# Kernel tuning notes

Measured on AMD Instinct MI355X. Metric: run time of the kernel, lower is better.

## Reference

```python
import jax, jax.numpy as jnp
import numpy as np
from jax import lax

# Topology constants (windowed DAG: compute node i, at global index N_IN+i,
# reads the FANIN immediately preceding global node values).
N_IN = 16      # number of input nodes
FANIN = 16     # connections per compute node
N_NODES = 512  # topologically ordered compute nodes (hidden + output)
N_OUT = 64     # last N_OUT nodes in node_order are outputs
BATCH = 32768
T = N_IN + N_NODES  # total node count


def setup_inputs() -> dict:
    key = jax.random.key(0)
    k1, k2, k3, k4 = jax.random.split(key, 4)
    x = jax.random.normal(k1, (BATCH, N_IN), dtype=jnp.float32)
    # weights scaled down so tanh is not fully saturated through 512 layers
    weights = jax.random.normal(k2, (N_NODES, FANIN), dtype=jnp.float32) * 0.25
    biases = jax.random.normal(k3, (N_NODES,), dtype=jnp.float32) * 0.1
    responses = 1.0 + 0.1 * jax.random.normal(k4, (N_NODES,), dtype=jnp.float32)
    # src indices for node i: global indices [i, i+FANIN) (== previous FANIN nodes,
    # since N_IN == FANIN). Shape [N_NODES, FANIN], int32, all in [0, T).
    src_idx = (jnp.arange(N_NODES, dtype=jnp.int32)[:, None]
               + jnp.arange(FANIN, dtype=jnp.int32)[None, :]
               + (N_IN - FANIN))
    return {"x": x, "weights": weights, "biases": biases,
            "responses": responses, "src_idx": src_idx}


def _forward(x, weights, biases, responses, src_idx):
    B = x.shape[0]
    # values buffer [B, T]: inputs first, then compute nodes in topo order
    values0 = jnp.zeros((B, T), dtype=x.dtype).at[:, :N_IN].set(x)

    def body(values, xs):
        i, idx_row, w, b, r = xs
        src_vals = jnp.take(values, idx_row, axis=1)        # [B, FANIN] gather
        agg = src_vals @ w                                   # [B] weighted sum
        out = jnp.tanh(agg + b) * r                          # activation
        values = lax.dynamic_update_slice(values, out[:, None], (0, N_IN + i))
        return values, None

    ii = jnp.arange(N_NODES, dtype=jnp.int32)
    values, _ = lax.scan(body, values0, (ii, src_idx, weights, biases, responses))
    return values[:, T - N_OUT:]  # [B, N_OUT]


def reference(x, weights, biases, responses, src_idx):
    return _forward(x, weights, biases, responses, src_idx)
```

## Files before the change

kernel.cpp:

```cpp
#include <hip/hip_runtime.h>


typedef float v4f __attribute__((ext_vector_type(4)));

constexpr int kNodes  = 512;
constexpr int kNOut   = 64;
constexpr int kBatch  = 32768;
constexpr int kStrideF = 20;
constexpr int kLdsFloats = (kNodes + 3) * kStrideF + 4;
constexpr float kScale = 2.8853900817779268f;

#define PREF(S) {                                                             \
    asm volatile(                                                             \
      "ds_read_b128 %0, %5 offset:0\n\t"                                      \
      "ds_read_b128 %1, %5 offset:16\n\t"                                     \
      "ds_read_b128 %2, %5 offset:32\n\t"                                     \
      "ds_read_b128 %3, %5 offset:48\n\t"                                     \
      "ds_read_b128 %4, %5 offset:64"                                         \
      : "=&v"(q0[S]), "=&v"(q1[S]), "=&v"(q2[S]), "=&v"(q3[S]), "=&v"(q4[S])  \
      : "v"(a));                                                              \
    a += kStrideF * 4; }

#define WAITQ(S)                                                              \
    asm volatile("s_waitcnt lgkmcnt(15)"                                      \
      : "+v"(q0[S]), "+v"(q1[S]), "+v"(q2[S]), "+v"(q3[S]), "+v"(q4[S]));

#define NODE(K, A0,A1,A2,A3,A4,A5,A6,A7,A8,A9,A10,A11,A12,A13,A14,A15) {     \
    PREF(((K)+3)&3)                                                          \
    WAITQ((K)&3)                                                             \
    const int s = (K)&3;                                                     \
    v4f qa = q0[s], qb = q1[s], qc = q2[s], qd = q3[s], qm = q4[s];          \
    float p0 = fmaf(A0,  qa.x, qm.x);                                        \
    float p1 = A4  * qb.x;                                                   \
    float p2 = A8  * qc.x;                                                   \
    float p3 = A12 * qd.x;                                                   \
    p0 = fmaf(A1,  qa.y, p0);  p1 = fmaf(A5,  qb.y, p1);                     \
    p2 = fmaf(A9,  qc.y, p2);  p3 = fmaf(A13, qd.y, p3);                     \
    p0 = fmaf(A2,  qa.z, p0);  p1 = fmaf(A6,  qb.z, p1);                     \
    p2 = fmaf(A10, qc.z, p2);  p3 = fmaf(A14, qd.z, p3);                     \
    p0 = fmaf(A3,  qa.w, p0);  p1 = fmaf(A7,  qb.w, p1);                     \
    p2 = fmaf(A11, qc.w, p2);                                                \
    float pre = (p0 + p1) + (p2 + p3);                                       \
    float acc = fmaf(A15, qd.w, pre);          \
    float e = __builtin_amdgcn_exp2f(acc);                                   \
    float u = __builtin_amdgcn_rcpf(e + 1.0f);                               \
    A0 = fmaf(qm.z, u, qm.y); }

__global__ __launch_bounds__(128) void neat_fwd(
    const float* __restrict__ x,
    const float* __restrict__ w,
    const float* __restrict__ bias,
    const float* __restrict__ resp,
    float* __restrict__ out)
{
    __shared__ float lds[kLdsFloats];

    const int t = threadIdx.x;

    const float4* __restrict__ w4 = reinterpret_cast<const float4*>(w);
    #pragma unroll
    for (int j = 0; j < 16; ++j) {
        int i4 = t + j * 128;
        float4 v = w4[i4];
        int node = i4 >> 2, pos = (i4 & 3) << 2;
        float4 s = make_float4(v.x * kScale, v.y * kScale, v.z * kScale, v.w * kScale);
        *reinterpret_cast<float4*>(lds + node * kStrideF + pos) = s;
    }
    #pragma unroll
    for (int j = 0; j < 4; ++j) {
        int n = t + j * 128;
        float b = bias[n], r = resp[n];
        lds[n * kStrideF + 16] = b * kScale;
        lds[n * kStrideF + 17] = r;
        lds[n * kStrideF + 18] = -2.0f * r;
        lds[n * kStrideF + 19] = 0.0f;
    }

    const int b = blockIdx.x * blockDim.x + t;
    const float4* __restrict__ x4 = reinterpret_cast<const float4*>(x) + (size_t)b * 4;
    float4 a0 = x4[0], a1 = x4[1], a2 = x4[2], a3 = x4[3];
    float v0  = a0.x, v1  = a0.y, v2  = a0.z, v3  = a0.w;
    float v4  = a1.x, v5  = a1.y, v6  = a1.z, v7  = a1.w;
    float v8  = a2.x, v9  = a2.y, v10 = a2.z, v11 = a2.w;
    float v12 = a3.x, v13 = a3.y, v14 = a3.z, v15 = a3.w;

    float* __restrict__ op = out + (size_t)b * kNOut;

    __syncthreads();

    unsigned int a = (unsigned int)(unsigned long long)(&lds[0]);

    v4f q0[4], q1[4], q2[4], q3[4], q4[4];
    PREF(0) PREF(1) PREF(2)

    #pragma unroll 1
    for (int g = 0; g < 32; ++g) {
        NODE( 0, v0 ,v1 ,v2 ,v3 ,v4 ,v5 ,v6 ,v7 ,v8 ,v9 ,v10,v11,v12,v13,v14,v15)
        NODE( 1, v1 ,v2 ,v3 ,v4 ,v5 ,v6 ,v7 ,v8 ,v9 ,v10,v11,v12,v13,v14,v15,v0 )
        NODE( 2, v2 ,v3 ,v4 ,v5 ,v6 ,v7 ,v8 ,v9 ,v10,v11,v12,v13,v14,v15,v0 ,v1 )
        NODE( 3, v3 ,v4 ,v5 ,v6 ,v7 ,v8 ,v9 ,v10,v11,v12,v13,v14,v15,v0 ,v1 ,v2 )
        NODE( 4, v4 ,v5 ,v6 ,v7 ,v8 ,v9 ,v10,v11,v12,v13,v14,v15,v0 ,v1 ,v2 ,v3 )
        NODE( 5, v5 ,v6 ,v7 ,v8 ,v9 ,v10,v11,v12,v13,v14,v15,v0 ,v1 ,v2 ,v3 ,v4 )
        NODE( 6, v6 ,v7 ,v8 ,v9 ,v10,v11,v12,v13,v14,v15,v0 ,v1 ,v2 ,v3 ,v4 ,v5 )
        NODE( 7, v7 ,v8 ,v9 ,v10,v11,v12,v13,v14,v15,v0 ,v1 ,v2 ,v3 ,v4 ,v5 ,v6 )
        NODE( 8, v8 ,v9 ,v10,v11,v12,v13,v14,v15,v0 ,v1 ,v2 ,v3 ,v4 ,v5 ,v6 ,v7 )
        NODE( 9, v9 ,v10,v11,v12,v13,v14,v15,v0 ,v1 ,v2 ,v3 ,v4 ,v5 ,v6 ,v7 ,v8 )
        NODE(10, v10,v11,v12,v13,v14,v15,v0 ,v1 ,v2 ,v3 ,v4 ,v5 ,v6 ,v7 ,v8 ,v9 )
        NODE(11, v11,v12,v13,v14,v15,v0 ,v1 ,v2 ,v3 ,v4 ,v5 ,v6 ,v7 ,v8 ,v9 ,v10)
        NODE(12, v12,v13,v14,v15,v0 ,v1 ,v2 ,v3 ,v4 ,v5 ,v6 ,v7 ,v8 ,v9 ,v10,v11)
        NODE(13, v13,v14,v15,v0 ,v1 ,v2 ,v3 ,v4 ,v5 ,v6 ,v7 ,v8 ,v9 ,v10,v11,v12)
        NODE(14, v14,v15,v0 ,v1 ,v2 ,v3 ,v4 ,v5 ,v6 ,v7 ,v8 ,v9 ,v10,v11,v12,v13)
        NODE(15, v15,v0 ,v1 ,v2 ,v3 ,v4 ,v5 ,v6 ,v7 ,v8 ,v9 ,v10,v11,v12,v13,v14)
        if (g >= 28) {
            float4* o4 = reinterpret_cast<float4*>(op + (g - 28) * 16);
            o4[0] = make_float4(v0,  v1,  v2,  v3);
            o4[1] = make_float4(v4,  v5,  v6,  v7);
            o4[2] = make_float4(v8,  v9,  v10, v11);
            o4[3] = make_float4(v12, v13, v14, v15);
        }
    }

    asm volatile("s_waitcnt lgkmcnt(0)" ::: "memory");
}

extern "C" void kernel_launch(void* const* d_in, const int* in_sizes, int n_in,
                              void* d_out, int out_size, void* d_ws, size_t ws_size,
                              hipStream_t stream) {
    const float* x    = (const float*)d_in[0];
    const float* w    = (const float*)d_in[1];
    const float* bias = (const float*)d_in[2];
    const float* resp = (const float*)d_in[3];
    float* out = (float*)d_out;
    dim3 block(128);
    dim3 grid(kBatch / 128);
    hipLaunchKernelGGL(neat_fwd, grid, block, 0, stream, x, w, bias, resp, out);
}
```

Before: 99.88 us.

## Split each batch row across four lanes with DPP reductions and folded response scaling

Each batch element is now handled by a quad of four lanes, each holding 4 of the 16 sliding-window values and computing a partial dot product. The partials are combined with DPP quad permutes, and the window is rotated across lanes with a DPP shift. Response factors are folded into the downstream weights in LDS, and the final outputs are rescaled by the response at store time. This gives four times as many threads and more latency hiding per row, at the cost of a per-node cross-lane reduction and redundant exp/rcp work in every lane of the quad.

```diff
diff --git a/kernel.cpp b/kernel.cpp
--- a/kernel.cpp
+++ b/kernel.cpp
@@ -3,120 +3,121 @@
 
 typedef float v4f __attribute__((ext_vector_type(4)));
 
-constexpr int kNodes  = 512;
-constexpr int kNOut   = 64;
-constexpr int kBatch  = 32768;
-constexpr int kStrideF = 20;
-constexpr int kLdsFloats = (kNodes + 3) * kStrideF + 4;
-constexpr float kScale = 2.8853900817779268f;
+constexpr int kNOut     = 64;
+constexpr int kBatch    = 32768;
+constexpr int kQStrideF = 80;
+constexpr int kLdsFloats = (128 + 3) * kQStrideF;
+constexpr float kScale  = 2.8853900817779268f;
 
-#define PREF(S) {                                                             \
+#define QPERM(X, CTRL) __int_as_float(__builtin_amdgcn_update_dpp(            \
+    __float_as_int(X), __float_as_int(X), (CTRL), 0xF, 0xF, false))
+
+#define PREFQ(S) {                                                            \
     asm volatile(                                                             \
       "ds_read_b128 %0, %5 offset:0\n\t"                                      \
-      "ds_read_b128 %1, %5 offset:16\n\t"                                     \
-      "ds_read_b128 %2, %5 offset:32\n\t"                                     \
-      "ds_read_b128 %3, %5 offset:48\n\t"                                     \
-      "ds_read_b128 %4, %5 offset:64"                                         \
-      : "=&v"(q0[S]), "=&v"(q1[S]), "=&v"(q2[S]), "=&v"(q3[S]), "=&v"(q4[S])  \
+      "ds_read_b128 %1, %5 offset:64\n\t"                                     \
+      "ds_read_b128 %2, %5 offset:128\n\t"                                    \
+      "ds_read_b128 %3, %5 offset:192\n\t"                                    \
+      "ds_read_b128 %4, %5 offset:256"                                        \
+      : "=&v"(qw0[S]), "=&v"(qw1[S]), "=&v"(qw2[S]), "=&v"(qw3[S]),           \
+        "=&v"(qb[S])                                                          \
       : "v"(a));                                                              \
-    a += kStrideF * 4; }
+    a += kQStrideF * 4; }
 
 #define WAITQ(S)                                                              \
     asm volatile("s_waitcnt lgkmcnt(15)"                                      \
-      : "+v"(q0[S]), "+v"(q1[S]), "+v"(q2[S]), "+v"(q3[S]), "+v"(q4[S]));
+      : "+v"(qw0[S]), "+v"(qw1[S]), "+v"(qw2[S]), "+v"(qw3[S]), "+v"(qb[S]));
 
-#define NODE(K, A0,A1,A2,A3,A4,A5,A6,A7,A8,A9,A10,A11,A12,A13,A14,A15) {     \
-    PREF(((K)+3)&3)                                                          \
-    WAITQ((K)&3)                                                             \
-    const int s = (K)&3;                                                     \
-    v4f qa = q0[s], qb = q1[s], qc = q2[s], qd = q3[s], qm = q4[s];          \
-    float p0 = fmaf(A0,  qa.x, qm.x);                                        \
-    float p1 = A4  * qb.x;                                                   \
-    float p2 = A8  * qc.x;                                                   \
-    float p3 = A12 * qd.x;                                                   \
-    p0 = fmaf(A1,  qa.y, p0);  p1 = fmaf(A5,  qb.y, p1);                     \
-    p2 = fmaf(A9,  qc.y, p2);  p3 = fmaf(A13, qd.y, p3);                     \
-    p0 = fmaf(A2,  qa.z, p0);  p1 = fmaf(A6,  qb.z, p1);                     \
-    p2 = fmaf(A10, qc.z, p2);  p3 = fmaf(A14, qd.z, p3);                     \
-    p0 = fmaf(A3,  qa.w, p0);  p1 = fmaf(A7,  qb.w, p1);                     \
-    p2 = fmaf(A11, qc.w, p2);                                                \
-    float pre = (p0 + p1) + (p2 + p3);                                       \
-    float acc = fmaf(A15, qd.w, pre);          \
-    float e = __builtin_amdgcn_exp2f(acc);                                   \
-    float u = __builtin_amdgcn_rcpf(e + 1.0f);                               \
-    A0 = fmaf(qm.z, u, qm.y); }
+#define NODE1(QW, BSV, WA, WB, WC, WD) {                                      \
+    float ini = is_l0 ? (BSV) : 0.0f;                                         \
+    float p = fmaf((WA), (QW).x, ini);                                        \
+    p = fmaf((WB), (QW).y, p);                                                \
+    p = fmaf((WC), (QW).z, p);                                                \
+    p = fmaf((WD), (QW).w, p);                                                \
+    float s1 = p + QPERM(p, 0xB1);                   \
+    float sf = s1 + QPERM(s1, 0x4E);                 \
+    float ex = __builtin_amdgcn_exp2f(sf);                                    \
+    float uu = __builtin_amdgcn_rcpf(ex + 1.0f);                              \
+    float tn = fmaf(-2.0f, uu, 1.0f);             \
+    float mg = QPERM((WA), 0x39);                    \
+    (WA) = is_l3 ? tn : mg; }
 
-__global__ __launch_bounds__(128) void neat_fwd(
+#define NODEQ(S) {                                                            \
+    PREFQ(((S) + 3) & 3)                                                      \
+    WAITQ(S)                                                                  \
+    v4f f0 = qw0[S], f1 = qw1[S], f2 = qw2[S], f3 = qw3[S], fb = qb[S];       \
+    NODE1(f0, fb.x, r0, r1, r2, r3)                                           \
+    NODE1(f1, fb.y, r1, r2, r3, r0)                                           \
+    NODE1(f2, fb.z, r2, r3, r0, r1)                                           \
+    NODE1(f3, fb.w, r3, r0, r1, r2) }
+
+__global__ __launch_bounds__(512) void neat_fwd(
     const float* __restrict__ x,
     const float* __restrict__ w,
     const float* __restrict__ bias,
     const float* __restrict__ resp,
     float* __restrict__ out)
 {
-    __shared__ float lds[kLdsFloats];
+    __shared__ alignas(16) float ldsw[kLdsFloats];
+    __shared__ float rst[512];
 
-    const int t = threadIdx.x;
+    const int t  = threadIdx.x;
+    const int jl = t & 3;
+    const bool is_l0 = (jl == 0);
+    const bool is_l3 = (jl == 3);
+
+    rst[t] = resp[t];
+    __syncthreads();
 
     const float4* __restrict__ w4 = reinterpret_cast<const float4*>(w);
     #pragma unroll
-    for (int j = 0; j < 16; ++j) {
-        int i4 = t + j * 128;
+    for (int k = 0; k < 4; ++k) {
+        int i4 = t + k * 512;
         float4 v = w4[i4];
-        int node = i4 >> 2, pos = (i4 & 3) << 2;
-        float4 s = make_float4(v.x * kScale, v.y * kScale, v.z * kScale, v.w * kScale);
-        *reinterpret_cast<float4*>(lds + node * kStrideF + pos) = s;
+        int n = i4 >> 2, k4 = i4 & 3;
+        int s0 = n + 4 * k4;
+        float f0 = kScale * ((s0 + 0 < 16) ? 1.0f : rst[s0 - 16]);
+        float f1 = kScale * ((s0 + 1 < 16) ? 1.0f : rst[s0 - 15]);
+        float f2 = kScale * ((s0 + 2 < 16) ? 1.0f : rst[s0 - 14]);
+        float f3 = kScale * ((s0 + 3 < 16) ? 1.0f : rst[s0 - 13]);
+        float4 sc = make_float4(v.x * f0, v.y * f1, v.z * f2, v.w * f3);
+        *reinterpret_cast<float4*>(
+            &ldsw[(n >> 2) * kQStrideF + (n & 3) * 16 + k4 * 4]) = sc;
     }
-    #pragma unroll
-    for (int j = 0; j < 4; ++j) {
-        int n = t + j * 128;
-        float b = bias[n], r = resp[n];
-        lds[n * kStrideF + 16] = b * kScale;
-        lds[n * kStrideF + 17] = r;
-        lds[n * kStrideF + 18] = -2.0f * r;
-        lds[n * kStrideF + 19] = 0.0f;
+    {
+        float bs = bias[t] * kScale;
+        int q = t >> 2, s = t & 3;
+        #pragma unroll
+        for (int rep = 0; rep < 4; ++rep)
+            ldsw[q * kQStrideF + 64 + rep * 4 + s] = bs;
     }
 
-    const int b = blockIdx.x * blockDim.x + t;
-    const float4* __restrict__ x4 = reinterpret_cast<const float4*>(x) + (size_t)b * 4;
-    float4 a0 = x4[0], a1 = x4[1], a2 = x4[2], a3 = x4[3];
-    float v0  = a0.x, v1  = a0.y, v2  = a0.z, v3  = a0.w;
-    float v4  = a1.x, v5  = a1.y, v6  = a1.z, v7  = a1.w;
-    float v8  = a2.x, v9  = a2.y, v10 = a2.z, v11 = a2.w;
-    float v12 = a3.x, v13 = a3.y, v14 = a3.z, v15 = a3.w;
+    const int e = blockIdx.x * 128 + (t >> 2);
+    const float4 xi = reinterpret_cast<const float4*>(x)[e * 4 + jl];
+    float r0 = xi.x, r1 = xi.y, r2 = xi.z, r3 = xi.w;
 
-    float* __restrict__ op = out + (size_t)b * kNOut;
+    const float4* __restrict__ rr4 = reinterpret_cast<const float4*>(resp);
+    const float4 rv0 = rr4[112 + jl], rv1 = rr4[116 + jl],
+                 rv2 = rr4[120 + jl], rv3 = rr4[124 + jl];
+
+    float* __restrict__ op = out + (size_t)e * kNOut + jl * 4;
 
     __syncthreads();
 
-    unsigned int a = (unsigned int)(unsigned long long)(&lds[0]);
+    unsigned int a = (unsigned int)(unsigned long long)(&ldsw[0])
+                   + (unsigned int)(jl << 4);
 
-    v4f q0[4], q1[4], q2[4], q3[4], q4[4];
-    PREF(0) PREF(1) PREF(2)
+    v4f qw0[4], qw1[4], qw2[4], qw3[4], qb[4];
+    PREFQ(0) PREFQ(1) PREFQ(2)
 
     #pragma unroll 1
     for (int g = 0; g < 32; ++g) {
-        NODE( 0, v0 ,v1 ,v2 ,v3 ,v4 ,v5 ,v6 ,v7 ,v8 ,v9 ,v10,v11,v12,v13,v14,v15)
-        NODE( 1, v1 ,v2 ,v3 ,v4 ,v5 ,v6 ,v7 ,v8 ,v9 ,v10,v11,v12,v13,v14,v15,v0 )
-        NODE( 2, v2 ,v3 ,v4 ,v5 ,v6 ,v7 ,v8 ,v9 ,v10,v11,v12,v13,v14,v15,v0 ,v1 )
-        NODE( 3, v3 ,v4 ,v5 ,v6 ,v7 ,v8 ,v9 ,v10,v11,v12,v13,v14,v15,v0 ,v1 ,v2 )
-        NODE( 4, v4 ,v5 ,v6 ,v7 ,v8 ,v9 ,v10,v11,v12,v13,v14,v15,v0 ,v1 ,v2 ,v3 )
-        NODE( 5, v5 ,v6 ,v7 ,v8 ,v9 ,v10,v11,v12,v13,v14,v15,v0 ,v1 ,v2 ,v3 ,v4 )
-        NODE( 6, v6 ,v7 ,v8 ,v9 ,v10,v11,v12,v13,v14,v15,v0 ,v1 ,v2 ,v3 ,v4 ,v5 )
-        NODE( 7, v7 ,v8 ,v9 ,v10,v11,v12,v13,v14,v15,v0 ,v1 ,v2 ,v3 ,v4 ,v5 ,v6 )
-        NODE( 8, v8 ,v9 ,v10,v11,v12,v13,v14,v15,v0 ,v1 ,v2 ,v3 ,v4 ,v5 ,v6 ,v7 )
-        NODE( 9, v9 ,v10,v11,v12,v13,v14,v15,v0 ,v1 ,v2 ,v3 ,v4 ,v5 ,v6 ,v7 ,v8 )
-        NODE(10, v10,v11,v12,v13,v14,v15,v0 ,v1 ,v2 ,v3 ,v4 ,v5 ,v6 ,v7 ,v8 ,v9 )
-        NODE(11, v11,v12,v13,v14,v15,v0 ,v1 ,v2 ,v3 ,v4 ,v5 ,v6 ,v7 ,v8 ,v9 ,v10)
-        NODE(12, v12,v13,v14,v15,v0 ,v1 ,v2 ,v3 ,v4 ,v5 ,v6 ,v7 ,v8 ,v9 ,v10,v11)
-        NODE(13, v13,v14,v15,v0 ,v1 ,v2 ,v3 ,v4 ,v5 ,v6 ,v7 ,v8 ,v9 ,v10,v11,v12)
-        NODE(14, v14,v15,v0 ,v1 ,v2 ,v3 ,v4 ,v5 ,v6 ,v7 ,v8 ,v9 ,v10,v11,v12,v13)
-        NODE(15, v15,v0 ,v1 ,v2 ,v3 ,v4 ,v5 ,v6 ,v7 ,v8 ,v9 ,v10,v11,v12,v13,v14)
+        NODEQ(0) NODEQ(1) NODEQ(2) NODEQ(3)
         if (g >= 28) {
-            float4* o4 = reinterpret_cast<float4*>(op + (g - 28) * 16);
-            o4[0] = make_float4(v0,  v1,  v2,  v3);
-            o4[1] = make_float4(v4,  v5,  v6,  v7);
-            o4[2] = make_float4(v8,  v9,  v10, v11);
-            o4[3] = make_float4(v12, v13, v14, v15);
+            float4 rv = (g == 28) ? rv0 : (g == 29) ? rv1
+                      : (g == 30) ? rv2 : rv3;
+            *reinterpret_cast<float4*>(op + (g - 28) * 16) =
+                make_float4(r0 * rv.x, r1 * rv.y, r2 * rv.z, r3 * rv.w);
         }
     }
 
@@ -131,7 +132,7 @@
     const float* bias = (const float*)d_in[2];
     const float* resp = (const float*)d_in[3];
     float* out = (float*)d_out;
-    dim3 block(128);
-    dim3 grid(kBatch / 128);
+    dim3 block(512);
+    dim3 grid((kBatch * 4) / 512);
     hipLaunchKernelGGL(neat_fwd, grid, block, 0, stream, x, w, bias, resp, out);
 }
```

New measurement: 101.2 us. About the same (+1.3%).
